# Kernel optimization log

Hardware: AMD Instinct MI355X
Metric: run time of the kernel (lower is better)

Reference implementation:

```python
import jax, jax.numpy as jnp
import numpy as np

N = 100000       # nodes
E = 1600000      # edges (avg degree 16)
F_IN, HID, C, K = 64, 64, 16, 3


def setup_inputs() -> dict:
    key = jax.random.key(0)
    ks = jax.random.split(key, 4)
    x = jax.random.normal(ks[0], (N, F_IN), dtype=jnp.float32)
    edge_index = jax.random.randint(ks[1], (2, E), 0, N, dtype=jnp.int32)
    s1 = 1.0 / np.sqrt(F_IN)
    W1 = jax.random.uniform(ks[2], (K, F_IN, HID), jnp.float32, -s1, s1)
    b1 = jnp.zeros((HID,), jnp.float32)
    s2 = 1.0 / np.sqrt(HID)
    W2 = jax.random.uniform(ks[3], (K, HID, C), jnp.float32, -s2, s2)
    b2 = jnp.zeros((C,), jnp.float32)
    return {"x": x, "edge_index": edge_index, "W1": W1, "b1": b1, "W2": W2, "b2": b2}


def _cheb_conv(x, row, col, wedge, W, b):
    """PyG ChebConv with sym norm, lambda_max=2: L_hat = -D^-1/2 A D^-1/2."""
    prop = lambda h: jax.ops.segment_sum(h[col] * wedge[:, None], row, num_segments=N)
    Tx0 = x
    out = Tx0 @ W[0]
    Tx1 = prop(x)
    out = out + Tx1 @ W[1]
    for k in range(2, W.shape[0]):
        Tx2 = 2.0 * prop(Tx1) - Tx0
        out = out + Tx2 @ W[k]
        Tx0, Tx1 = Tx1, Tx2
    return out + b


def reference(x, edge_index, W1, b1, W2, b2):
    row, col = edge_index[0], edge_index[1]
    deg = jax.ops.segment_sum(jnp.ones((edge_index.shape[1],), x.dtype), row, num_segments=N)
    dinv = jnp.where(deg > 0, jax.lax.rsqrt(jnp.maximum(deg, 1.0)), 0.0)
    wedge = -dinv[row] * dinv[col]  # scaled-Laplacian edge weights
    h = jax.nn.relu(_cheb_conv(x, row, col, wedge, W1, b1))
    # dropout: identity in eval mode
    out = _cheb_conv(h, row, col, wedge, W2, b2)
    return jax.nn.log_softmax(out, axis=1)
```

## Files before the change

kernel.cpp:

```cpp
#include <hip/hip_runtime.h>

#define NN 100000
#define NE 1600000
#define NBUCK 391
#define CAP 5632

typedef __attribute__((ext_vector_type(8))) short bf16x8;
typedef __attribute__((ext_vector_type(4))) short bf16x4;
typedef __attribute__((ext_vector_type(4))) float f32x4;

__device__ inline unsigned short f2bf(float f) {
    unsigned int u = __float_as_uint(f);
    return (unsigned short)((u + 0x7FFFu + ((u >> 16) & 1u)) >> 16);
}
__device__ inline float bf2f(short s) {
    return __uint_as_float(((unsigned int)(unsigned short)s) << 16);
}

__global__ __launch_bounds__(256) void k_bin(const int* __restrict__ row, const int* __restrict__ col,
                                             int* __restrict__ gcursor, int* __restrict__ ebuf) {
    __shared__ int hist[NBUCK];
    for (int i = threadIdx.x; i < NBUCK; i += 256) hist[i] = 0;
    __syncthreads();
    int start = blockIdx.x * 3125;
    int end = start + 3125; if (end > NE) end = NE;
    for (int e = start + threadIdx.x; e < end; e += 256)
        atomicAdd(&hist[row[e] >> 8], 1);
    __syncthreads();
    for (int i = threadIdx.x; i < NBUCK; i += 256)
        hist[i] = atomicAdd(&gcursor[i], hist[i]);
    __syncthreads();
    for (int e = start + threadIdx.x; e < end; e += 256) {
        int r = row[e], c = col[e];
        int bk = r >> 8;
        int pos = atomicAdd(&hist[bk], 1);
        if (pos < CAP) ebuf[bk * CAP + pos] = (c << 8) | (r & 255);
    }
}

__global__ void k_bstart(const int* __restrict__ gcursor, int* __restrict__ bstart,
                         int* __restrict__ row_ptr) {
    __shared__ int s[512];
    int t = threadIdx.x;
    int d = (t < NBUCK) ? gcursor[t] : 0;
    s[t] = d; __syncthreads();
    for (int off = 1; off < 512; off <<= 1) {
        int v = (t >= off) ? s[t - off] : 0;
        __syncthreads();
        s[t] += v;
        __syncthreads();
    }
    if (t < NBUCK) bstart[t] = s[t] - d;
    if (t == NBUCK - 1) bstart[NBUCK] = s[t];
    if (t == 0) row_ptr[NN] = NE;
}

__global__ __launch_bounds__(256) void k_build(const int* __restrict__ ebuf, const int* __restrict__ bstart,
                                               int* __restrict__ row_ptr, float* __restrict__ dinv,
                                               float* __restrict__ rdeg, int* __restrict__ col_sorted) {
    __shared__ int deg[256], cur[256], ps[256];
    int b = blockIdx.x;
    int bs = bstart[b], cnt = bstart[b + 1] - bs;
    const int* eb = ebuf + (size_t)b * CAP;
    int t = threadIdx.x;
    deg[t] = 0;
    __syncthreads();
    for (int e = t; e < cnt; e += 256)
        atomicAdd(&deg[eb[e] & 255], 1);
    __syncthreads();
    int d = deg[t];
    ps[t] = d; __syncthreads();
    for (int off = 1; off < 256; off <<= 1) {
        int v = (t >= off) ? ps[t - off] : 0;
        __syncthreads();
        ps[t] += v;
        __syncthreads();
    }
    int base = bs + ps[t] - d;
    cur[t] = base;
    int n = (b << 8) + t;
    if (n < NN) {
        row_ptr[n] = base;
        dinv[n] = d > 0 ? rsqrtf((float)d) : 0.f;
        rdeg[n] = sqrtf((float)d);
    }
    __syncthreads();
    for (int e = t; e < cnt; e += 256) {
        int w = eb[e];
        int pos = atomicAdd(&cur[w & 255], 1);
        col_sorted[pos] = ((unsigned)w) >> 8;
    }
}

__global__ void k_scale(const float* __restrict__ x, const float* __restrict__ dinv,
                        unsigned short* __restrict__ xsbf, unsigned short* __restrict__ xbf) {
    int t = blockIdx.x * 256 + threadIdx.x;
    if (t < NN * 16) {
        float d = dinv[t >> 4];
        f32x4 v = ((const f32x4*)x)[t];
        bf16x4 u, s;
        u[0] = (short)f2bf(v[0]); u[1] = (short)f2bf(v[1]); u[2] = (short)f2bf(v[2]); u[3] = (short)f2bf(v[3]);
        s[0] = (short)f2bf(v[0] * d); s[1] = (short)f2bf(v[1] * d); s[2] = (short)f2bf(v[2] * d); s[3] = (short)f2bf(v[3] * d);
        ((bf16x4*)xbf)[t] = u;
        ((bf16x4*)xsbf)[t] = s;
    }
}

__global__ __launch_bounds__(256) void k_spmm64b(const unsigned short* __restrict__ ins,
                                                 const unsigned short* __restrict__ subbf,
                                                 unsigned short* __restrict__ outb,
                                                 unsigned short* __restrict__ outsb,
                                                 const int* __restrict__ row_ptr, const int* __restrict__ cs,
                                                 const float* __restrict__ dinv,
                                                 int has_sub, int has_outb, int has_outs) {
    int n = blockIdx.x * 4 + (threadIdx.x >> 6);
    if (n >= NN) return;
    int nu = __builtin_amdgcn_readfirstlane(n);
    int lane = threadIdx.x & 63;
    int es = lane >> 3;
    int f = lane & 7;
    int s = row_ptr[nu], e = row_ptr[nu + 1];
    float a0[8] = {0,0,0,0,0,0,0,0}, a1[8] = {0,0,0,0,0,0,0,0};
    int i = s;
    for (; i + 15 < e; i += 16) {
        int c0 = cs[i + es];
        int c1 = cs[i + 8 + es];
        bf16x8 v0 = *((const bf16x8*)(ins + (size_t)c0 * 64 + f * 8));
        bf16x8 v1 = *((const bf16x8*)(ins + (size_t)c1 * 64 + f * 8));
        #pragma unroll
        for (int j = 0; j < 8; ++j) { a0[j] += bf2f(v0[j]); a1[j] += bf2f(v1[j]); }
    }
    for (; i + es < e; i += 8) {
        int c0 = cs[i + es];
        bf16x8 v0 = *((const bf16x8*)(ins + (size_t)c0 * 64 + f * 8));
        #pragma unroll
        for (int j = 0; j < 8; ++j) a0[j] += bf2f(v0[j]);
    }
    float a[8];
    #pragma unroll
    for (int j = 0; j < 8; ++j) {
        a[j] = a0[j] + a1[j];
        a[j] += __shfl_xor(a[j], 8);
        a[j] += __shfl_xor(a[j], 16);
        a[j] += __shfl_xor(a[j], 32);
    }
    if (es == 0) {
        float dn = dinv[nu];
        float r[8];
        #pragma unroll
        for (int j = 0; j < 8; ++j) r[j] = -dn * a[j];
        if (has_sub) {
            bf16x8 sv = *((const bf16x8*)(subbf + (size_t)nu * 64 + f * 8));
            #pragma unroll
            for (int j = 0; j < 8; ++j) r[j] = 2.f * r[j] - bf2f(sv[j]);
        }
        if (has_outb) {
            bf16x8 ob;
            #pragma unroll
            for (int j = 0; j < 8; ++j) ob[j] = (short)f2bf(r[j]);
            *((bf16x8*)(outb + (size_t)nu * 64 + f * 8)) = ob;
        }
        if (has_outs) {
            bf16x8 os;
            #pragma unroll
            for (int j = 0; j < 8; ++j) os[j] = (short)f2bf(dn * r[j]);
            *((bf16x8*)(outsb + (size_t)nu * 64 + f * 8)) = os;
        }
    }
}

__global__ __launch_bounds__(256) void k_d1p(const unsigned short* __restrict__ xbf,
                                             const unsigned short* __restrict__ t1s,
                                             const unsigned short* __restrict__ t2bf,
                                             const float* __restrict__ W1, const float* __restrict__ b1,
                                             const float* __restrict__ W2, const float* __restrict__ b2,
                                             const float* __restrict__ dinv, const float* __restrict__ rdeg,
                                             unsigned short* __restrict__ Apreb, unsigned short* __restrict__ Gsb) {
    __shared__ unsigned short Wf1[24 * 64 * 8];
    __shared__ unsigned short Wf2[6 * 64 * 8];
    __shared__ unsigned short Ht[4][1024];
    for (int slot = threadIdx.x; slot < 24 * 64; slot += 256) {
        int c = slot / 384;
        int t = (slot / 64) % 6;
        int l = slot & 63;
        int rr = l & 15, gg = l >> 4;
        unsigned int pk[4];
        #pragma unroll
        for (int jp = 0; jp < 4; ++jp) {
            int k0 = t * 32 + gg * 8 + jp * 2;
            unsigned int lo = f2bf(W1[(k0 >> 6) * 4096 + (k0 & 63) * 64 + c * 16 + rr]);
            int k1 = k0 + 1;
            unsigned int hi = f2bf(W1[(k1 >> 6) * 4096 + (k1 & 63) * 64 + c * 16 + rr]);
            pk[jp] = lo | (hi << 16);
        }
        *((uint4*)&Wf1[slot * 8]) = *((uint4*)pk);
    }
    for (int slot = threadIdx.x; slot < 6 * 64; slot += 256) {
        int c = slot / 128;
        int t = (slot / 64) & 1;
        int l = slot & 63;
        int rr = l & 15, gg = l >> 4;
        unsigned int pk[4];
        #pragma unroll
        for (int jp = 0; jp < 4; ++jp) {
            int k0 = t * 32 + gg * 8 + jp * 2;
            int k1 = k0 + 1;
            float w0, w1;
            if (c == 0)      { w0 = W2[k0 * 16 + rr] - W2[2048 + k0 * 16 + rr];
                               w1 = W2[k1 * 16 + rr] - W2[2048 + k1 * 16 + rr]; }
            else if (c == 1) { w0 = W2[1024 + k0 * 16 + rr]; w1 = W2[1024 + k1 * 16 + rr]; }
            else             { w0 = W2[2048 + k0 * 16 + rr]; w1 = W2[2048 + k1 * 16 + rr]; }
            pk[jp] = (unsigned int)f2bf(w0) | ((unsigned int)f2bf(w1) << 16);
        }
        *((uint4*)&Wf2[slot * 8]) = *((uint4*)pk);
    }
    __syncthreads();

    int lane = threadIdx.x & 63;
    int r = lane & 15, g = lane >> 4;
    int widx = threadIdx.x >> 6;
    char* ht = (char*)Ht[widx];

    bf16x8 bfr1[4][6];
    #pragma unroll
    for (int c = 0; c < 4; ++c)
        #pragma unroll
        for (int t = 0; t < 6; ++t)
            bfr1[c][t] = *((const bf16x8*)&Wf1[((c * 6 + t) * 64 + lane) * 8]);
    bf16x8 bfr2[3][2];
    #pragma unroll
    for (int c = 0; c < 3; ++c)
        #pragma unroll
        for (int t = 0; t < 2; ++t)
            bfr2[c][t] = *((const bf16x8*)&Wf2[((c * 2 + t) * 64 + lane) * 8]);

    float bl[4];
    #pragma unroll
    for (int c = 0; c < 4; ++c) bl[c] = b1[c * 16 + r];
    float b2r = b2[r];

    const unsigned short* arrs[3] = {xbf, t1s, t2bf};
    int wid = blockIdx.x * 4 + widx;
    int wstride = gridDim.x * 4;
    for (int tile = wid; tile < NN / 16; tile += wstride) {
        int nb = tile * 16;
        bf16x8 af[6];
        #pragma unroll
        for (int t = 0; t < 6; ++t)
            af[t] = *((const bf16x8*)(arrs[t >> 1] + (size_t)(nb + r) * 64 + (t & 1) * 32 + g * 8));
        f32x4 acc[4], accT[4];
        #pragma unroll
        for (int c = 0; c < 4; ++c) {
            acc[c] = (f32x4){bl[c], bl[c], bl[c], bl[c]};
            accT[c] = (f32x4){0.f, 0.f, 0.f, 0.f};
        }
        #pragma unroll
        for (int c = 0; c < 4; ++c) {
            acc[c]  = __builtin_amdgcn_mfma_f32_16x16x32_bf16(af[0], bfr1[c][0], acc[c], 0, 0, 0);
            acc[c]  = __builtin_amdgcn_mfma_f32_16x16x32_bf16(af[1], bfr1[c][1], acc[c], 0, 0, 0);
            accT[c] = __builtin_amdgcn_mfma_f32_16x16x32_bf16(af[2], bfr1[c][2], accT[c], 0, 0, 0);
            accT[c] = __builtin_amdgcn_mfma_f32_16x16x32_bf16(af[3], bfr1[c][3], accT[c], 0, 0, 0);
            acc[c]  = __builtin_amdgcn_mfma_f32_16x16x32_bf16(af[4], bfr1[c][4], acc[c], 0, 0, 0);
            acc[c]  = __builtin_amdgcn_mfma_f32_16x16x32_bf16(af[5], bfr1[c][5], acc[c], 0, 0, 0);
        }
        float rdq[4];
        #pragma unroll
        for (int q = 0; q < 4; ++q) rdq[q] = rdeg[nb + g * 4 + q];
        #pragma unroll
        for (int c = 0; c < 4; ++c)
            #pragma unroll
            for (int q = 0; q < 4; ++q) {
                float hval = fmaxf(acc[c][q] + rdq[q] * accT[c][q], 0.f);
                int node = g * 4 + q;
                int byte = (node * 64 + c * 16 + r) * 2;
                byte ^= (node & 7) << 4;
                *((unsigned short*)(ht + byte)) = f2bf(hval);
            }
        bf16x8 af2[2];
        #pragma unroll
        for (int t = 0; t < 2; ++t) {
            int byte = (r * 64 + t * 32 + g * 8) * 2;
            byte ^= (r & 7) << 4;
            af2[t] = *((const bf16x8*)(ht + byte));
        }
        f32x4 acc2[3];
        #pragma unroll
        for (int c = 0; c < 3; ++c) acc2[c] = (f32x4){0.f, 0.f, 0.f, 0.f};
        #pragma unroll
        for (int t = 0; t < 2; ++t)
            #pragma unroll
            for (int c = 0; c < 3; ++c)
                acc2[c] = __builtin_amdgcn_mfma_f32_16x16x32_bf16(af2[t], bfr2[c][t], acc2[c], 0, 0, 0);
        #pragma unroll
        for (int q = 0; q < 4; ++q) {
            int n = nb + g * 4 + q;
            float dv = dinv[n];
            Apreb[(size_t)n * 16 + r] = f2bf(acc2[0][q] + b2r);
            Gsb[(size_t)n * 32 + r]      = f2bf(acc2[1][q] * dv);
            Gsb[(size_t)n * 32 + 16 + r] = f2bf(acc2[2][q] * dv);
        }
    }
}

__global__ __launch_bounds__(256) void k_spmm32b(const unsigned short* __restrict__ Gsb,
                                                 unsigned short* __restrict__ q1b, unsigned short* __restrict__ tsb,
                                                 const int* __restrict__ row_ptr, const int* __restrict__ cs,
                                                 const float* __restrict__ dinv) {
    int n = blockIdx.x * 4 + (threadIdx.x >> 6);
    if (n >= NN) return;
    int nu = __builtin_amdgcn_readfirstlane(n);
    int lane = threadIdx.x & 63;
    int es = lane >> 3;
    int f = lane & 7;
    int s = row_ptr[nu], e = row_ptr[nu + 1];
    float a0[4] = {0,0,0,0}, a1[4] = {0,0,0,0};
    int i = s;
    for (; i + 15 < e; i += 16) {
        int c0 = cs[i + es];
        int c1 = cs[i + 8 + es];
        bf16x4 v0 = *((const bf16x4*)(Gsb + (size_t)c0 * 32 + f * 4));
        bf16x4 v1 = *((const bf16x4*)(Gsb + (size_t)c1 * 32 + f * 4));
        #pragma unroll
        for (int j = 0; j < 4; ++j) { a0[j] += bf2f(v0[j]); a1[j] += bf2f(v1[j]); }
    }
    for (; i + es < e; i += 8) {
        int c0 = cs[i + es];
        bf16x4 v0 = *((const bf16x4*)(Gsb + (size_t)c0 * 32 + f * 4));
        #pragma unroll
        for (int j = 0; j < 4; ++j) a0[j] += bf2f(v0[j]);
    }
    float a[4];
    #pragma unroll
    for (int j = 0; j < 4; ++j) {
        a[j] = a0[j] + a1[j];
        a[j] += __shfl_xor(a[j], 8);
        a[j] += __shfl_xor(a[j], 16);
        a[j] += __shfl_xor(a[j], 32);
    }
    if (es == 0) {
        float dn = dinv[nu];
        if (f < 4) {
            bf16x4 w;
            #pragma unroll
            for (int j = 0; j < 4; ++j) w[j] = (short)f2bf(-dn * a[j]);
            *((bf16x4*)(q1b + (size_t)nu * 16 + f * 4)) = w;
        } else {
            bf16x4 w;
            #pragma unroll
            for (int j = 0; j < 4; ++j) w[j] = (short)f2bf(dn * (-dn * a[j]));
            *((bf16x4*)(tsb + (size_t)nu * 16 + (f - 4) * 4)) = w;
        }
    }
}

__global__ __launch_bounds__(256) void k_spmm16f(const unsigned short* __restrict__ tsb,
                                                 const unsigned short* __restrict__ Apreb,
                                                 const unsigned short* __restrict__ q1b,
                                                 const int* __restrict__ row_ptr, const int* __restrict__ cs,
                                                 const float* __restrict__ dinv, float* __restrict__ out) {
    int n = blockIdx.x * 4 + (threadIdx.x >> 6);
    if (n >= NN) return;
    int nu = __builtin_amdgcn_readfirstlane(n);
    int lane = threadIdx.x & 63;
    int es = lane >> 2;
    int f = lane & 3;
    int s = row_ptr[nu], e = row_ptr[nu + 1];
    float a0[4] = {0,0,0,0}, a1[4] = {0,0,0,0};
    int i = s;
    for (; i + 31 < e; i += 32) {
        int c0 = cs[i + es];
        int c1 = cs[i + 16 + es];
        bf16x4 v0 = *((const bf16x4*)(tsb + (size_t)c0 * 16 + f * 4));
        bf16x4 v1 = *((const bf16x4*)(tsb + (size_t)c1 * 16 + f * 4));
        #pragma unroll
        for (int j = 0; j < 4; ++j) { a0[j] += bf2f(v0[j]); a1[j] += bf2f(v1[j]); }
    }
    for (; i + es < e; i += 16) {
        int c0 = cs[i + es];
        bf16x4 v0 = *((const bf16x4*)(tsb + (size_t)c0 * 16 + f * 4));
        #pragma unroll
        for (int j = 0; j < 4; ++j) a0[j] += bf2f(v0[j]);
    }
    float a[4];
    #pragma unroll
    for (int j = 0; j < 4; ++j) {
        a[j] = a0[j] + a1[j];
        a[j] += __shfl_xor(a[j], 4);
        a[j] += __shfl_xor(a[j], 8);
        a[j] += __shfl_xor(a[j], 16);
        a[j] += __shfl_xor(a[j], 32);
    }
    if (es == 0) {
        float dn = dinv[nu];
        bf16x4 ap = *((const bf16x4*)(Apreb + (size_t)nu * 16 + f * 4));
        bf16x4 qv = *((const bf16x4*)(q1b + (size_t)nu * 16 + f * 4));
        float o[4];
        #pragma unroll
        for (int j = 0; j < 4; ++j)
            o[j] = bf2f(ap[j]) + bf2f(qv[j]) + 2.f * (-dn * a[j]);
        float m = fmaxf(fmaxf(o[0], o[1]), fmaxf(o[2], o[3]));
        m = fmaxf(m, __shfl_xor(m, 1));
        m = fmaxf(m, __shfl_xor(m, 2));
        float ssum = expf(o[0] - m) + expf(o[1] - m) + expf(o[2] - m) + expf(o[3] - m);
        ssum += __shfl_xor(ssum, 1);
        ssum += __shfl_xor(ssum, 2);
        float ls = logf(ssum);
        f32x4 w;
        w[0] = o[0] - m - ls; w[1] = o[1] - m - ls; w[2] = o[2] - m - ls; w[3] = o[3] - m - ls;
        *((f32x4*)(out + (size_t)nu * 16 + f * 4)) = w;
    }
}

extern "C" void kernel_launch(void* const* d_in, const int* in_sizes, int n_in,
                              void* d_out, int out_size, void* d_ws, size_t ws_size,
                              hipStream_t stream) {
    const float* x  = (const float*)d_in[0];
    const int*   ei = (const int*)d_in[1];
    const int*   row = ei;
    const int*   col = ei + NE;
    const float* W1 = (const float*)d_in[2];
    const float* b1 = (const float*)d_in[3];
    const float* W2 = (const float*)d_in[4];
    const float* b2 = (const float*)d_in[5];
    float* out = (float*)d_out;

    char* base = (char*)d_ws;
    size_t off = 0;
    auto alloc = [&](size_t bytes) -> char* {
        char* r = base + off;
        off = (off + bytes + 255) & ~(size_t)255;
        return r;
    };
    int*   gcursor    = (int*)alloc(NBUCK * 4);
    int*   bstart     = (int*)alloc((NBUCK + 1) * 4);
    float* dinv       = (float*)alloc((size_t)NN * 4);
    float* rdeg       = (float*)alloc((size_t)NN * 4);
    int*   row_ptr    = (int*)alloc((size_t)(NN + 1) * 4);
    int*   ebuf       = (int*)alloc((size_t)NBUCK * CAP * 4);
    int*   col_sorted = (int*)alloc((size_t)NE * 4);
    unsigned short* Xbf  = (unsigned short*)alloc((size_t)NN * 64 * 2);
    unsigned short* XSbf = (unsigned short*)alloc((size_t)NN * 64 * 2);
    unsigned short* T1s  = (unsigned short*)alloc((size_t)NN * 64 * 2);
    unsigned short* T2bf = (unsigned short*)alloc((size_t)NN * 64 * 2);
    unsigned short* Apreb = (unsigned short*)alloc((size_t)NN * 16 * 2);
    unsigned short* Gsb  = (unsigned short*)alloc((size_t)NN * 32 * 2);
    unsigned short* q1b  = (unsigned short*)alloc((size_t)NN * 16 * 2);
    unsigned short* tsb  = (unsigned short*)alloc((size_t)NN * 16 * 2);

    hipMemsetAsync(gcursor, 0, NBUCK * 4, stream);

    k_bin<<<512, 256, 0, stream>>>(row, col, gcursor, ebuf);
    k_bstart<<<1, 512, 0, stream>>>(gcursor, bstart, row_ptr);
    k_build<<<NBUCK, 256, 0, stream>>>(ebuf, bstart, row_ptr, dinv, rdeg, col_sorted);
    k_scale<<<(NN * 16 + 255) / 256, 256, 0, stream>>>(x, dinv, XSbf, Xbf);

    int nbS = (NN + 3) / 4;
    k_spmm64b<<<nbS, 256, 0, stream>>>(XSbf, nullptr, nullptr, T1s, row_ptr, col_sorted, dinv, 0, 0, 1);
    k_spmm64b<<<nbS, 256, 0, stream>>>(T1s, Xbf, T2bf, nullptr, row_ptr, col_sorted, dinv, 1, 1, 0);
    k_d1p<<<625, 256, 0, stream>>>(Xbf, T1s, T2bf, W1, b1, W2, b2, dinv, rdeg, Apreb, Gsb);
    k_spmm32b<<<nbS, 256, 0, stream>>>(Gsb, q1b, tsb, row_ptr, col_sorted, dinv);
    k_spmm16f<<<nbS, 256, 0, stream>>>(tsb, Apreb, q1b, row_ptr, col_sorted, dinv, out);
}
```

Baseline: 233.6 us.

## Fuse second 64-wide SpMM into dense MFMA kernel and fold bucket scan into build

The second Chebyshev propagation (T2 = 2·L·T1 − X) now runs inside the dense layer kernel. Each 16-node block gathers its rows into a swizzled LDS tile and feeds them straight into the MFMA layer-1 and layer-2 products, so the T2 intermediate is never written to or read back from global memory. The separate single-block bucket prefix-scan kernel is removed, and every build block recomputes the scan redundantly in shared memory, saving one launch. In exchange, the fused kernel reloads the weights into LDS in each of 6250 blocks instead of 625 persistent ones. Its gather phase may also have poorer occupancy and load balance than the standalone SpMM.

```diff
diff --git a/kernel.cpp b/kernel.cpp
--- a/kernel.cpp
+++ b/kernel.cpp
@@ -38,31 +38,30 @@
     }
 }
 
-__global__ void k_bstart(const int* __restrict__ gcursor, int* __restrict__ bstart,
-                         int* __restrict__ row_ptr) {
-    __shared__ int s[512];
-    int t = threadIdx.x;
-    int d = (t < NBUCK) ? gcursor[t] : 0;
-    s[t] = d; __syncthreads();
-    for (int off = 1; off < 512; off <<= 1) {
-        int v = (t >= off) ? s[t - off] : 0;
-        __syncthreads();
-        s[t] += v;
-        __syncthreads();
-    }
-    if (t < NBUCK) bstart[t] = s[t] - d;
-    if (t == NBUCK - 1) bstart[NBUCK] = s[t];
-    if (t == 0) row_ptr[NN] = NE;
-}
-
-__global__ __launch_bounds__(256) void k_build(const int* __restrict__ ebuf, const int* __restrict__ bstart,
+__global__ __launch_bounds__(256) void k_build(const int* __restrict__ ebuf, const int* __restrict__ gcursor,
                                                int* __restrict__ row_ptr, float* __restrict__ dinv,
                                                float* __restrict__ rdeg, int* __restrict__ col_sorted) {
     __shared__ int deg[256], cur[256], ps[256];
+    __shared__ int bsL[NBUCK + 1];
+    int t = threadIdx.x;
+    int d0 = (2 * t < NBUCK) ? gcursor[2 * t] : 0;
+    int d1 = (2 * t + 1 < NBUCK) ? gcursor[2 * t + 1] : 0;
+    ps[t] = d0 + d1;
+    __syncthreads();
+    for (int off = 1; off < 256; off <<= 1) {
+        int v = (t >= off) ? ps[t - off] : 0;
+        __syncthreads();
+        ps[t] += v;
+        __syncthreads();
+    }
+    int ex = ps[t] - d0 - d1;
+    if (2 * t < NBUCK) bsL[2 * t] = ex;
+    if (2 * t + 1 < NBUCK) bsL[2 * t + 1] = ex + d0;
+    __syncthreads();
     int b = blockIdx.x;
-    int bs = bstart[b], cnt = bstart[b + 1] - bs;
+    int bs = bsL[b];
+    int cnt = gcursor[b];
     const int* eb = ebuf + (size_t)b * CAP;
-    int t = threadIdx.x;
     deg[t] = 0;
     __syncthreads();
     for (int e = t; e < cnt; e += 256)
@@ -84,6 +83,7 @@
         dinv[n] = d > 0 ? rsqrtf((float)d) : 0.f;
         rdeg[n] = sqrtf((float)d);
     }
+    if (b == 0 && t == 0) row_ptr[NN] = NE;
     __syncthreads();
     for (int e = t; e < cnt; e += 256) {
         int w = eb[e];
@@ -107,12 +107,9 @@
 }
 
 __global__ __launch_bounds__(256) void k_spmm64b(const unsigned short* __restrict__ ins,
-                                                 const unsigned short* __restrict__ subbf,
-                                                 unsigned short* __restrict__ outb,
                                                  unsigned short* __restrict__ outsb,
                                                  const int* __restrict__ row_ptr, const int* __restrict__ cs,
-                                                 const float* __restrict__ dinv,
-                                                 int has_sub, int has_outb, int has_outs) {
+                                                 const float* __restrict__ dinv) {
     int n = blockIdx.x * 4 + (threadIdx.x >> 6);
     if (n >= NN) return;
     int nu = __builtin_amdgcn_readfirstlane(n);
@@ -146,39 +143,24 @@
     }
     if (es == 0) {
         float dn = dinv[nu];
-        float r[8];
-        #pragma unroll
-        for (int j = 0; j < 8; ++j) r[j] = -dn * a[j];
-        if (has_sub) {
-            bf16x8 sv = *((const bf16x8*)(subbf + (size_t)nu * 64 + f * 8));
-            #pragma unroll
-            for (int j = 0; j < 8; ++j) r[j] = 2.f * r[j] - bf2f(sv[j]);
-        }
-        if (has_outb) {
-            bf16x8 ob;
-            #pragma unroll
-            for (int j = 0; j < 8; ++j) ob[j] = (short)f2bf(r[j]);
-            *((bf16x8*)(outb + (size_t)nu * 64 + f * 8)) = ob;
-        }
-        if (has_outs) {
-            bf16x8 os;
-            #pragma unroll
-            for (int j = 0; j < 8; ++j) os[j] = (short)f2bf(dn * r[j]);
-            *((bf16x8*)(outsb + (size_t)nu * 64 + f * 8)) = os;
-        }
-    }
-}
-
-__global__ __launch_bounds__(256) void k_d1p(const unsigned short* __restrict__ xbf,
-                                             const unsigned short* __restrict__ t1s,
-                                             const unsigned short* __restrict__ t2bf,
-                                             const float* __restrict__ W1, const float* __restrict__ b1,
-                                             const float* __restrict__ W2, const float* __restrict__ b2,
-                                             const float* __restrict__ dinv, const float* __restrict__ rdeg,
-                                             unsigned short* __restrict__ Apreb, unsigned short* __restrict__ Gsb) {
+        bf16x8 os;
+        #pragma unroll
+        for (int j = 0; j < 8; ++j) os[j] = (short)f2bf(dn * (-dn * a[j]));
+        *((bf16x8*)(outsb + (size_t)nu * 64 + f * 8)) = os;
+    }
+}
+
+__global__ __launch_bounds__(256) void k_fuse(const unsigned short* __restrict__ xbf,
+                                              const unsigned short* __restrict__ t1s,
+                                              const float* __restrict__ W1, const float* __restrict__ b1,
+                                              const float* __restrict__ W2, const float* __restrict__ b2,
+                                              const float* __restrict__ dinv, const float* __restrict__ rdeg,
+                                              const int* __restrict__ row_ptr, const int* __restrict__ cs,
+                                              unsigned short* __restrict__ Apreb, unsigned short* __restrict__ Gsb) {
     __shared__ unsigned short Wf1[24 * 64 * 8];
     __shared__ unsigned short Wf2[6 * 64 * 8];
-    __shared__ unsigned short Ht[4][1024];
+    __shared__ unsigned short T2t[16 * 64];
+    __shared__ unsigned short Htile[16 * 64];
     for (int slot = threadIdx.x; slot < 24 * 64; slot += 256) {
         int c = slot / 384;
         int t = (slot / 64) % 6;
@@ -214,90 +196,111 @@
         }
         *((uint4*)&Wf2[slot * 8]) = *((uint4*)pk);
     }
-    __syncthreads();
 
     int lane = threadIdx.x & 63;
+    int widx = threadIdx.x >> 6;
     int r = lane & 15, g = lane >> 4;
-    int widx = threadIdx.x >> 6;
-    char* ht = (char*)Ht[widx];
-
-    bf16x8 bfr1[4][6];
-    #pragma unroll
-    for (int c = 0; c < 4; ++c)
-        #pragma unroll
-        for (int t = 0; t < 6; ++t)
-            bfr1[c][t] = *((const bf16x8*)&Wf1[((c * 6 + t) * 64 + lane) * 8]);
-    bf16x8 bfr2[3][2];
-    #pragma unroll
-    for (int c = 0; c < 3; ++c)
+    int nb = blockIdx.x * 16;
+
+    int es = lane >> 3, fq = lane & 7;
+    #pragma unroll
+    for (int q = 0; q < 4; ++q) {
+        int n = nb + widx * 4 + q;
+        int s = row_ptr[n], e = row_ptr[n + 1];
+        float a0[8] = {0,0,0,0,0,0,0,0}, a1[8] = {0,0,0,0,0,0,0,0};
+        int i = s;
+        for (; i + 15 < e; i += 16) {
+            int c0 = cs[i + es];
+            int c1 = cs[i + 8 + es];
+            bf16x8 v0 = *((const bf16x8*)(t1s + (size_t)c0 * 64 + fq * 8));
+            bf16x8 v1 = *((const bf16x8*)(t1s + (size_t)c1 * 64 + fq * 8));
+            #pragma unroll
+            for (int j = 0; j < 8; ++j) { a0[j] += bf2f(v0[j]); a1[j] += bf2f(v1[j]); }
+        }
+        for (; i + es < e; i += 8) {
+            int c0 = cs[i + es];
+            bf16x8 v0 = *((const bf16x8*)(t1s + (size_t)c0 * 64 + fq * 8));
+            #pragma unroll
+            for (int j = 0; j < 8; ++j) a0[j] += bf2f(v0[j]);
+        }
+        float a[8];
+        #pragma unroll
+        for (int j = 0; j < 8; ++j) {
+            a[j] = a0[j] + a1[j];
+            a[j] += __shfl_xor(a[j], 8);
+            a[j] += __shfl_xor(a[j], 16);
+            a[j] += __shfl_xor(a[j], 32);
+        }
+        if (es == 0) {
+            float dn = dinv[n];
+            bf16x8 xv = *((const bf16x8*)(xbf + (size_t)n * 64 + fq * 8));
+            bf16x8 ob;
+            #pragma unroll
+            for (int j = 0; j < 8; ++j)
+                ob[j] = (short)f2bf(2.f * (-dn * a[j]) - bf2f(xv[j]));
+            int ln = widx * 4 + q;
+            int byte = (ln * 128 + fq * 16) ^ ((ln & 7) << 4);
+            *((bf16x8*)((char*)T2t + byte)) = ob;
+        }
+    }
+    __syncthreads();
+
+    bf16x8 bfr1[6];
+    #pragma unroll
+    for (int t = 0; t < 6; ++t)
+        bfr1[t] = *((const bf16x8*)&Wf1[((widx * 6 + t) * 64 + lane) * 8]);
+    float bl = b1[widx * 16 + r];
+
+    bf16x8 af[6];
+    af[0] = *((const bf16x8*)(xbf + (size_t)(nb + r) * 64 + g * 8));
+    af[1] = *((const bf16x8*)(xbf + (size_t)(nb + r) * 64 + 32 + g * 8));
+    af[2] = *((const bf16x8*)(t1s + (size_t)(nb + r) * 64 + g * 8));
+    af[3] = *((const bf16x8*)(t1s + (size_t)(nb + r) * 64 + 32 + g * 8));
+    {
+        int byte0 = (r * 128 + g * 16) ^ ((r & 7) << 4);
+        int byte1 = (r * 128 + 64 + g * 16) ^ ((r & 7) << 4);
+        af[4] = *((const bf16x8*)((char*)T2t + byte0));
+        af[5] = *((const bf16x8*)((char*)T2t + byte1));
+    }
+    f32x4 acc = (f32x4){bl, bl, bl, bl};
+    f32x4 accT = (f32x4){0.f, 0.f, 0.f, 0.f};
+    acc  = __builtin_amdgcn_mfma_f32_16x16x32_bf16(af[0], bfr1[0], acc, 0, 0, 0);
+    acc  = __builtin_amdgcn_mfma_f32_16x16x32_bf16(af[1], bfr1[1], acc, 0, 0, 0);
+    accT = __builtin_amdgcn_mfma_f32_16x16x32_bf16(af[2], bfr1[2], accT, 0, 0, 0);
+    accT = __builtin_amdgcn_mfma_f32_16x16x32_bf16(af[3], bfr1[3], accT, 0, 0, 0);
+    acc  = __builtin_amdgcn_mfma_f32_16x16x32_bf16(af[4], bfr1[4], acc, 0, 0, 0);
+    acc  = __builtin_amdgcn_mfma_f32_16x16x32_bf16(af[5], bfr1[5], acc, 0, 0, 0);
+    #pragma unroll
+    for (int q = 0; q < 4; ++q) {
+        int node = g * 4 + q;
+        float hval = fmaxf(acc[q] + rdeg[nb + node] * accT[q], 0.f);
+        int byte = (node * 128 + (widx * 16 + r) * 2) ^ ((node & 7) << 4);
+        *((unsigned short*)((char*)Htile + byte)) = f2bf(hval);
+    }
+    __syncthreads();
+
+    if (widx < 3) {
+        bf16x8 bfr2[2];
         #pragma unroll
         for (int t = 0; t < 2; ++t)
-            bfr2[c][t] = *((const bf16x8*)&Wf2[((c * 2 + t) * 64 + lane) * 8]);
-
-    float bl[4];
-    #pragma unroll
-    for (int c = 0; c < 4; ++c) bl[c] = b1[c * 16 + r];
-    float b2r = b2[r];
-
-    const unsigned short* arrs[3] = {xbf, t1s, t2bf};
-    int wid = blockIdx.x * 4 + widx;
-    int wstride = gridDim.x * 4;
-    for (int tile = wid; tile < NN / 16; tile += wstride) {
-        int nb = tile * 16;
-        bf16x8 af[6];
-        #pragma unroll
-        for (int t = 0; t < 6; ++t)
-            af[t] = *((const bf16x8*)(arrs[t >> 1] + (size_t)(nb + r) * 64 + (t & 1) * 32 + g * 8));
-        f32x4 acc[4], accT[4];
-        #pragma unroll
-        for (int c = 0; c < 4; ++c) {
-            acc[c] = (f32x4){bl[c], bl[c], bl[c], bl[c]};
-            accT[c] = (f32x4){0.f, 0.f, 0.f, 0.f};
-        }
-        #pragma unroll
-        for (int c = 0; c < 4; ++c) {
-            acc[c]  = __builtin_amdgcn_mfma_f32_16x16x32_bf16(af[0], bfr1[c][0], acc[c], 0, 0, 0);
-            acc[c]  = __builtin_amdgcn_mfma_f32_16x16x32_bf16(af[1], bfr1[c][1], acc[c], 0, 0, 0);
-            accT[c] = __builtin_amdgcn_mfma_f32_16x16x32_bf16(af[2], bfr1[c][2], accT[c], 0, 0, 0);
-            accT[c] = __builtin_amdgcn_mfma_f32_16x16x32_bf16(af[3], bfr1[c][3], accT[c], 0, 0, 0);
-            acc[c]  = __builtin_amdgcn_mfma_f32_16x16x32_bf16(af[4], bfr1[c][4], acc[c], 0, 0, 0);
-            acc[c]  = __builtin_amdgcn_mfma_f32_16x16x32_bf16(af[5], bfr1[c][5], acc[c], 0, 0, 0);
-        }
-        float rdq[4];
-        #pragma unroll
-        for (int q = 0; q < 4; ++q) rdq[q] = rdeg[nb + g * 4 + q];
-        #pragma unroll
-        for (int c = 0; c < 4; ++c)
-            #pragma unroll
-            for (int q = 0; q < 4; ++q) {
-                float hval = fmaxf(acc[c][q] + rdq[q] * accT[c][q], 0.f);
-                int node = g * 4 + q;
-                int byte = (node * 64 + c * 16 + r) * 2;
-                byte ^= (node & 7) << 4;
-                *((unsigned short*)(ht + byte)) = f2bf(hval);
-            }
+            bfr2[t] = *((const bf16x8*)&Wf2[((widx * 2 + t) * 64 + lane) * 8]);
         bf16x8 af2[2];
-        #pragma unroll
-        for (int t = 0; t < 2; ++t) {
-            int byte = (r * 64 + t * 32 + g * 8) * 2;
-            byte ^= (r & 7) << 4;
-            af2[t] = *((const bf16x8*)(ht + byte));
-        }
-        f32x4 acc2[3];
-        #pragma unroll
-        for (int c = 0; c < 3; ++c) acc2[c] = (f32x4){0.f, 0.f, 0.f, 0.f};
-        #pragma unroll
-        for (int t = 0; t < 2; ++t)
-            #pragma unroll
-            for (int c = 0; c < 3; ++c)
-                acc2[c] = __builtin_amdgcn_mfma_f32_16x16x32_bf16(af2[t], bfr2[c][t], acc2[c], 0, 0, 0);
+        {
+            int byte0 = (r * 128 + g * 16) ^ ((r & 7) << 4);
+            int byte1 = (r * 128 + 64 + g * 16) ^ ((r & 7) << 4);
+            af2[0] = *((const bf16x8*)((char*)Htile + byte0));
+            af2[1] = *((const bf16x8*)((char*)Htile + byte1));
+        }
+        f32x4 acc2 = (f32x4){0.f, 0.f, 0.f, 0.f};
+        acc2 = __builtin_amdgcn_mfma_f32_16x16x32_bf16(af2[0], bfr2[0], acc2, 0, 0, 0);
+        acc2 = __builtin_amdgcn_mfma_f32_16x16x32_bf16(af2[1], bfr2[1], acc2, 0, 0, 0);
+        float b2r = b2[r];
         #pragma unroll
         for (int q = 0; q < 4; ++q) {
             int n = nb + g * 4 + q;
-            float dv = dinv[n];
-            Apreb[(size_t)n * 16 + r] = f2bf(acc2[0][q] + b2r);
-            Gsb[(size_t)n * 32 + r]      = f2bf(acc2[1][q] * dv);
-            Gsb[(size_t)n * 32 + 16 + r] = f2bf(acc2[2][q] * dv);
+            if (widx == 0)      Apreb[(size_t)n * 16 + r] = f2bf(acc2[q] + b2r);
+            else if (widx == 1) Gsb[(size_t)n * 32 + r]      = f2bf(acc2[q] * dinv[n]);
+            else                Gsb[(size_t)n * 32 + 16 + r] = f2bf(acc2[q] * dinv[n]);
         }
     }
 }
@@ -432,7 +435,6 @@
         return r;
     };
     int*   gcursor    = (int*)alloc(NBUCK * 4);
-    int*   bstart     = (int*)alloc((NBUCK + 1) * 4);
     float* dinv       = (float*)alloc((size_t)NN * 4);
     float* rdeg       = (float*)alloc((size_t)NN * 4);
     int*   row_ptr    = (int*)alloc((size_t)(NN + 1) * 4);
@@ -441,7 +443,6 @@
     unsigned short* Xbf  = (unsigned short*)alloc((size_t)NN * 64 * 2);
     unsigned short* XSbf = (unsigned short*)alloc((size_t)NN * 64 * 2);
     unsigned short* T1s  = (unsigned short*)alloc((size_t)NN * 64 * 2);
-    unsigned short* T2bf = (unsigned short*)alloc((size_t)NN * 64 * 2);
     unsigned short* Apreb = (unsigned short*)alloc((size_t)NN * 16 * 2);
     unsigned short* Gsb  = (unsigned short*)alloc((size_t)NN * 32 * 2);
     unsigned short* q1b  = (unsigned short*)alloc((size_t)NN * 16 * 2);
@@ -450,14 +451,13 @@
     hipMemsetAsync(gcursor, 0, NBUCK * 4, stream);
 
     k_bin<<<512, 256, 0, stream>>>(row, col, gcursor, ebuf);
-    k_bstart<<<1, 512, 0, stream>>>(gcursor, bstart, row_ptr);
-    k_build<<<NBUCK, 256, 0, stream>>>(ebuf, bstart, row_ptr, dinv, rdeg, col_sorted);
+    k_build<<<NBUCK, 256, 0, stream>>>(ebuf, gcursor, row_ptr, dinv, rdeg, col_sorted);
     k_scale<<<(NN * 16 + 255) / 256, 256, 0, stream>>>(x, dinv, XSbf, Xbf);
 
     int nbS = (NN + 3) / 4;
-    k_spmm64b<<<nbS, 256, 0, stream>>>(XSbf, nullptr, nullptr, T1s, row_ptr, col_sorted, dinv, 0, 0, 1);
-    k_spmm64b<<<nbS, 256, 0, stream>>>(T1s, Xbf, T2bf, nullptr, row_ptr, col_sorted, dinv, 1, 1, 0);
-    k_d1p<<<625, 256, 0, stream>>>(Xbf, T1s, T2bf, W1, b1, W2, b2, dinv, rdeg, Apreb, Gsb);
+    k_spmm64b<<<nbS, 256, 0, stream>>>(XSbf, T1s, row_ptr, col_sorted, dinv);
+    k_fuse<<<NN / 16, 256, 0, stream>>>(Xbf, T1s, W1, b1, W2, b2, dinv, rdeg,
+                                        row_ptr, col_sorted, Apreb, Gsb);
     k_spmm32b<<<nbS, 256, 0, stream>>>(Gsb, q1b, tsb, row_ptr, col_sorted, dinv);
     k_spmm16f<<<nbS, 256, 0, stream>>>(tsb, Apreb, q1b, row_ptr, col_sorted, dinv, out);
 }
```

After: 277.0 us. 1.19x slower.
